# Kernel optimization log

Hardware: AMD Instinct MI355X
Metric: run time of the kernel (lower is better)

The kernel has to match this reference:

```python
import jax, jax.numpy as jnp
import numpy as np
from jax import lax

# hyperparams (match init_kwargs)
DIM = 192      # dim
QK = 192       # qk_dim
HEADS = 8
GS = 128       # group_size
MLP = 384      # mlp_dim
M = 64         # num_tokens
B, H, W = 4, 128, 128


def setup_inputs() -> dict:
    key = jax.random.key(0)
    ks = jax.random.split(key, 12)
    def n(k, sh, sc=0.02):
        return jax.random.normal(k, sh, dtype=jnp.float32) * sc
    return {
        "x": n(ks[0], (B, DIM, H, W), 1.0),
        "ln_g": jnp.ones((DIM,), jnp.float32),
        "ln_b": jnp.zeros((DIM,), jnp.float32),
        "Wq": n(ks[1], (DIM, QK)),
        "Wk": n(ks[2], (DIM, QK)),
        "Wv": n(ks[3], (DIM, DIM)),
        "Wproj": n(ks[4], (DIM, DIM)),
        "Wkg": n(ks[5], (DIM, QK)),      # IRCA global-key projection of means
        "Wvg": n(ks[6], (DIM, DIM)),     # IRCA global-value projection of means
        "means": n(ks[7], (M, DIM), 1.0),  # token dictionary buffer
        "Wconv": n(ks[8], (DIM, DIM)),   # 1x1 conv (no bias) as matrix
        "mlp_ln_g": jnp.ones((DIM,), jnp.float32),
        "mlp_ln_b": jnp.zeros((DIM,), jnp.float32),
        "W_fc1": n(ks[9], (DIM, MLP)),
        "dw": n(ks[10], (MLP, 1, 3, 3)),  # depthwise 3x3 in ConvFFN
        "W_fc2": n(ks[11], (MLP, DIM)),
    }


def _ln(x, g, b, eps=1e-5):
    mu = x.mean(-1, keepdims=True)
    var = ((x - mu) ** 2).mean(-1, keepdims=True)
    return (x - mu) * lax.rsqrt(var + eps) * g + b


def _attn(q, k, v):
    scale = q.shape[-1] ** -0.5
    s = jnp.einsum('...qd,...kd->...qk', q, k) * scale
    p = jax.nn.softmax(s, axis=-1)
    return jnp.einsum('...qk,...kd->...qd', p, v)


def reference(x, ln_g, ln_b, Wq, Wk, Wv, Wproj, Wkg, Wvg, means,
              Wconv, mlp_ln_g, mlp_ln_b, W_fc1, dw, W_fc2):
    b, C, h, w = x.shape
    N = h * w
    xt = x.reshape(b, C, N).transpose(0, 2, 1)          # b n c
    residual = xt
    xn = _ln(xt, ln_g, ln_b)

    # IRCA: per-head global K/V from the token dictionary (means)
    kg = (means @ Wkg).reshape(M, HEADS, QK // HEADS).transpose(1, 0, 2)   # h m dq
    vg = (means @ Wvg).reshape(M, HEADS, C // HEADS).transpose(1, 0, 2)    # h m dv

    # cluster assignment (no-grad): cosine sim to means, argsort by cluster id
    xs = lax.stop_gradient(xn)
    ms = lax.stop_gradient(means)
    xs_n = xs / (jnp.linalg.norm(xs, axis=-1, keepdims=True) + 1e-12)
    ms_n = ms / (jnp.linalg.norm(ms, axis=-1, keepdims=True) + 1e-12)
    belong = jnp.argmax(xs_n @ ms_n.T, axis=-1)          # b n
    idx = jnp.argsort(belong, axis=-1)                   # b n, cluster-sorted order

    # IASA: project, gather into cluster-sorted order
    q = jnp.take_along_axis(xn @ Wq, idx[:, :, None], axis=1)
    k = jnp.take_along_axis(xn @ Wk, idx[:, :, None], axis=1)
    v = jnp.take_along_axis(xn @ Wv, idx[:, :, None], axis=1)

    gs = min(N, GS)
    ng = (N + gs - 1) // gs
    pad_n = ng * gs - N
    pq = jnp.concatenate([q, q[:, N - pad_n:N][:, ::-1]], axis=1)
    pq = pq.reshape(b, ng, gs, HEADS, -1).transpose(0, 1, 3, 2, 4)  # b ng h gs dq

    def windows(t):
        tr = jnp.concatenate([t, t[:, N - pad_n - gs:N][:, ::-1]], axis=1)  # len ng*gs+gs
        t1 = tr[:, :ng * gs].reshape(b, ng, gs, -1)
        t2 = tr[:, gs:].reshape(b, ng, gs, -1)
        tw = jnp.concatenate([t1, t2], axis=2)           # b ng 2gs c
        return tw.reshape(b, ng, 2 * gs, HEADS, -1).transpose(0, 1, 3, 2, 4)

    kw, vw = windows(k), windows(v)
    out1 = _attn(pq, kw, vw)                             # local overlapping windows
    out2 = _attn(pq, kg[None, None], vg[None, None])     # global dictionary attention
    out = (out1 + out2).transpose(0, 1, 3, 2, 4).reshape(b, ng * gs, C)[:, :N]

    # scatter back to original token order (idx is a permutation)
    inv = jnp.argsort(idx, axis=-1)
    out = jnp.take_along_axis(out, inv[:, :, None], axis=1)
    out = (out @ Wproj) @ Wconv                           # proj + 1x1 conv (no bias)
    xt = residual + out

    # PreNorm ConvFFN: LN -> fc1 -> depthwise 3x3 -> GELU -> fc2, residual
    h1 = _ln(xt, mlp_ln_g, mlp_ln_b) @ W_fc1              # b n mlp
    himg = h1.transpose(0, 2, 1).reshape(b, MLP, h, w)
    dwc = lax.conv_general_dilated(himg, dw, (1, 1), 'SAME',
                                   feature_group_count=MLP,
                                   dimension_numbers=('NCHW', 'OIHW', 'NCHW'))
    h2 = jax.nn.gelu(dwc.reshape(b, MLP, N).transpose(0, 2, 1))
    xt = xt + h2 @ W_fc2
    return xt.transpose(0, 2, 1).reshape(b, C, h, w)
```

## Files before the change

### kernel.cpp

```cpp
#include <hip/hip_runtime.h>

using u16 = unsigned short;
using u32 = unsigned int;
typedef __attribute__((ext_vector_type(8))) short short8;
typedef __attribute__((ext_vector_type(4))) short s16x4;
typedef __attribute__((ext_vector_type(4))) float f32x4;
typedef __attribute__((ext_vector_type(2))) float f32x2;
typedef __attribute__((ext_vector_type(4))) u16 u16x4;
typedef __attribute__((ext_vector_type(4))) u32 u32x4;

constexpr int CB   = 4;
constexpr int CC   = 192;
constexpr int CN   = 16384;
constexpr int BN   = CB * CN;
constexpr int CMLP = 384;

__device__ __forceinline__ float b2f(u16 u){ return __uint_as_float(((u32)u) << 16); }
__device__ __forceinline__ u16 f2b(float f){
  u32 u = __float_as_uint(f);
  u32 r = (u + 0x7FFFu + ((u >> 16) & 1u)) >> 16;
  return (u16)r;
}
__device__ __forceinline__ short8 ld8(const u16* p) {
  s16x4 a = *(const s16x4*)p;
  s16x4 b = *(const s16x4*)(p + 4);
  short8 r;
  r[0]=a[0]; r[1]=a[1]; r[2]=a[2]; r[3]=a[3];
  r[4]=b[0]; r[5]=b[1]; r[6]=b[2]; r[7]=b[3];
  return r;
}
__device__ __forceinline__ u32 pk_bf16(float lo, float hi) {
  u32 r;
  asm("v_cvt_pk_bf16_f32 %0, %1, %2" : "=v"(r) : "v"(lo), "v"(hi));
  return r;
}
__device__ __forceinline__ float exp2_fast(float x) {
  float r;
  asm("v_exp_f32 %0, %1" : "=v"(r) : "v"(x));
  return r;
}
__device__ __forceinline__ void gl_lds16(const u16* g, u16* l) {
  __builtin_amdgcn_global_load_lds(
      (const __attribute__((address_space(1))) void*)(const void*)g,
      (__attribute__((address_space(3))) void*)(void*)l, 16, 0, 0);
}

template<int DOARG>
__global__ __launch_bounds__(256) void ln_k(const float* __restrict__ src,
    const float* __restrict__ gg, const float* __restrict__ bb, u16* __restrict__ out,
    const u16* __restrict__ msnT, int* __restrict__ belong)
{
  __shared__ float t[64 * 193];
  __shared__ float sg[192], sb[192];
  __shared__ float smu[64], srs[64];
  const int tid = threadIdx.x;
  const int blk = blockIdx.x;
  const int b = blk >> 8;
  const int n0 = (blk & 255) * 64;
  if (tid < 192) { sg[tid] = gg[tid]; sb[tid] = bb[tid]; }
  const size_t sbase = ((size_t)b * CC) * CN + n0;
  #pragma unroll
  for (int it = 0; it < 48; ++it) {
    int c = it * 4 + (tid >> 6);
    int tok = tid & 63;
    t[tok * 193 + c] = src[sbase + (size_t)c * CN + tok];
  }
  __syncthreads();
  {
    int tok = tid >> 2, sub = tid & 3;
    float s = 0.f, sq = 0.f;
    #pragma unroll
    for (int i = 0; i < 48; ++i) {
      float v = t[tok * 193 + sub * 48 + i];
      s += v; sq += v * v;
    }
    s  += __shfl_xor(s, 1);  s  += __shfl_xor(s, 2);
    sq += __shfl_xor(sq, 1); sq += __shfl_xor(sq, 2);
    float mu = s * (1.f / 192.f);
    float var = fmaxf(sq * (1.f / 192.f) - mu * mu, 0.f);
    float rs = rsqrtf(var + 1e-5f);
    if (sub == 0) { smu[tok] = mu; srs[tok] = rs; }
  }
  __syncthreads();
  const size_t obase = ((size_t)(b * CN + n0)) * CC;
  #pragma unroll
  for (int it = 0; it < 48; ++it) {
    int e = it * 256 + tid;
    int tk = e / 192, c = e % 192;
    float v = (t[tk * 193 + c] - smu[tk]) * srs[tk] * sg[c] + sb[c];
    out[obase + (size_t)tk * CC + c] = f2b(v);
  }

  if (DOARG) {
    const int wv = tid >> 6, lane = tid & 63;
    const int l15 = lane & 15, g4 = lane >> 4, q8 = g4 * 8;
    const int tok = wv * 16 + l15;
    const float mu = smu[tok], rs = srs[tok];
    short8 afm[6];
    #pragma unroll
    for (int ks = 0; ks < 6; ++ks) {
      u32x4 qq;
      #pragma unroll
      for (int j = 0; j < 4; ++j) {
        int c = ks * 32 + q8 + 2 * j;
        float v0 = (t[tok * 193 + c]     - mu) * rs * sg[c]     + sb[c];
        float v1 = (t[tok * 193 + c + 1] - mu) * rs * sg[c + 1] + sb[c + 1];
        qq[j] = pk_bf16(v0, v1);
      }
      afm[ks] = __builtin_bit_cast(short8, qq);
    }
    f32x4 sacc[4];
    #pragma unroll
    for (int ct = 0; ct < 4; ++ct) {
      sacc[ct] = 0.f;
      const u16* pM = msnT + (ct * 16 + l15) * 192 + q8;
      short8 mf[6];
      #pragma unroll
      for (int ks = 0; ks < 6; ++ks) mf[ks] = *(const short8*)(pM + ks * 32);
      #pragma unroll
      for (int ks = 0; ks < 6; ++ks)
        sacc[ct] = __builtin_amdgcn_mfma_f32_16x16x32_bf16(afm[ks], mf[ks], sacc[ct], 0, 0, 0);
    }
    #pragma unroll
    for (int r = 0; r < 4; ++r) {
      float bv = -3e38f; int bi = 1 << 30;
      #pragma unroll
      for (int ct = 0; ct < 4; ++ct) {
        float v = sacc[ct][r];
        int ci = ct * 16 + l15;
        if (v > bv || (v == bv && ci < bi)) { bv = v; bi = ci; }
      }
      #pragma unroll
      for (int d = 1; d < 16; d <<= 1) {
        float ov = __shfl_xor(bv, d);
        int   oi = __shfl_xor(bi, d);
        if (ov > bv || (ov == bv && oi < bi)) { bv = ov; bi = oi; }
      }
      if (l15 == 0) belong[b * CN + n0 + wv * 16 + g4 * 4 + r] = bi;
    }
  }
}

__global__ __launch_bounds__(192) void prep_means_k(const float* __restrict__ means,
    const float* __restrict__ Wkg, const float* __restrict__ Wvg,
    u16* __restrict__ msnT, float* __restrict__ kg, float* __restrict__ vg)
{
  __shared__ float sv[192];
  __shared__ float red[192];
  const int m = blockIdx.x, c = threadIdx.x;
  float v = means[m * 192 + c];
  sv[c] = v; red[c] = v * v;
  __syncthreads();
  for (int s = 96; s >= 3; s >>= 1) {
    if (c < s) red[c] += red[c + s];
    __syncthreads();
  }
  if (c == 0) red[0] = 1.f / (sqrtf(red[0] + red[1] + red[2]) + 1e-12f);
  __syncthreads();
  float scale = red[0];
  msnT[m * 192 + c] = f2b(v * scale);
  float a1 = 0.f, a2 = 0.f;
  for (int cc = 0; cc < 192; ++cc) {
    float mv = sv[cc];
    a1 += mv * Wkg[cc * 192 + c];
    a2 += mv * Wvg[cc * 192 + c];
  }
  int h = c / 24, d = c % 24;
  kg[h * (64 * 24) + m * 24 + d] = a1;
  vg[h * (64 * 24) + m * 24 + d] = a2;
}

__global__ __launch_bounds__(256) void wpcT_k(const float* __restrict__ Wp,
    const float* __restrict__ Wc, u16* __restrict__ WpcT)
{
  int e = blockIdx.x * 256 + threadIdx.x;
  if (e >= 192 * 192) return;
  int i = e / 192, j = e % 192;
  float a = 0.f;
  for (int k = 0; k < 192; ++k) a += Wp[i * 192 + k] * Wc[k * 192 + j];
  WpcT[j * 192 + i] = f2b(a);
}

__global__ __launch_bounds__(256) void wT_k(const float* __restrict__ W,
    u16* __restrict__ dst, int K, int NCsrc, int jcount)
{
  int e = blockIdx.x * 256 + threadIdx.x;
  if (e >= K * jcount) return;
  int j = e / K, k = e % K;
  dst[e] = f2b(W[k * NCsrc + j]);
}

enum { EP_QKV = 0, EP_RESID = 2, EP_H1 = 3, EP_FINAL = 4 };

template<int KTOT, int NCOLS, int EPI>
__global__ __launch_bounds__(256) void gemm3_k(const u16* __restrict__ A,
    const u16* __restrict__ Wt, const float* __restrict__ resid,
    void* __restrict__ outp, int astride,
    const float* __restrict__ g2, const float* __restrict__ b2, u16* __restrict__ ln2out)
{
  constexpr bool LNB = (EPI == EP_RESID);
  constexpr size_t SH_BYTES = LNB ? (size_t)(64 * 197 * 4) : (size_t)(64 * 192 * 2);
  __shared__ __attribute__((aligned(16))) char shraw[SH_BYTES];
  __shared__ float smu2[64], srs2[64];
  u16*   lA    = (u16*)shraw;
  float* lnbuf = (float*)shraw;
  constexpr int KC = KTOT / 192;
  constexpr int WCOLS = NCOLS / 4;
  constexpr int WCT = WCOLS / 16;
  constexpr int NACC = (KC == 2) ? WCT * 4 : 4;
  const int tid = threadIdx.x;
  const int row0 = blockIdx.y * 64;
  const int b = row0 >> 14;
  const int col0 = blockIdx.x * NCOLS;
  const int wv = tid >> 6, lane = tid & 63;
  const int l15 = lane & 15, g4 = lane >> 4, q8 = g4 * 8;
  const int colw = col0 + wv * WCOLS;

  f32x4 acc[NACC];
  #pragma unroll
  for (int i = 0; i < NACC; ++i) acc[i] = 0.f;

  #pragma unroll
  for (int kc = 0; kc < KC; ++kc) {
    if (kc) __syncthreads();
    #pragma unroll
    for (int j = 0; j < 6; ++j) {
      int C = (wv * 6 + j) * 64 + lane;
      int r = C / 24;
      int c = C - r * 24;
      const u16* gp = A + (size_t)(row0 + r) * astride + kc * 192 + c * 8;
      gl_lds16(gp, lA + (wv * 6 + j) * 512);
    }
    __syncthreads();
    short8 af[4][6];
    #pragma unroll
    for (int rt = 0; rt < 4; ++rt)
      #pragma unroll
      for (int ks = 0; ks < 6; ++ks)
        af[rt][ks] = *(const short8*)(lA + (rt * 16 + l15) * 192 + ks * 32 + q8);
    if (LNB) __syncthreads();

    #pragma unroll
    for (int jc = 0; jc < WCT; ++jc) {
      const u16* pW = Wt + (size_t)(colw + jc * 16 + l15) * KTOT + kc * 192 + q8;
      short8 wf[6];
      #pragma unroll
      for (int ks = 0; ks < 6; ++ks) wf[ks] = *(const short8*)(pW + ks * 32);
      #pragma unroll
      for (int ks = 0; ks < 6; ++ks)
        #pragma unroll
        for (int rt = 0; rt < 4; ++rt) {
          int ai = (KC == 2) ? jc * 4 + rt : rt;
          if (EPI == EP_FINAL || EPI == EP_RESID)
            acc[ai] = __builtin_amdgcn_mfma_f32_16x16x32_bf16(wf[ks], af[rt][ks], acc[ai], 0, 0, 0);
          else
            acc[ai] = __builtin_amdgcn_mfma_f32_16x16x32_bf16(af[rt][ks], wf[ks], acc[ai], 0, 0, 0);
        }

      if (KC == 1 && EPI == EP_QKV) {
        u16* o = (u16*)outp;
        int col = colw + jc * 16 + l15;
        #pragma unroll
        for (int rt = 0; rt < 4; ++rt) {
          int row = row0 + rt * 16 + g4 * 4;
          #pragma unroll
          for (int r = 0; r < 4; ++r)
            o[(size_t)(row + r) * 576 + col] = f2b(acc[rt][r]);
          acc[rt] = 0.f;
        }
      } else if (KC == 1 && EPI == EP_H1) {
        u16* o = (u16*)outp;
        int col = colw + jc * 16 + l15;
        #pragma unroll
        for (int rt = 0; rt < 4; ++rt) {
          int row = row0 + rt * 16 + g4 * 4;
          #pragma unroll
          for (int r = 0; r < 4; ++r)
            o[(size_t)(row + r) * CMLP + col] = f2b(acc[rt][r]);
          acc[rt] = 0.f;
        }
      } else if (KC == 1 && EPI == EP_RESID) {
        float* o = (float*)outp;
        #pragma unroll
        for (int rt = 0; rt < 4; ++rt) {
          int n = ((row0 + rt * 16) & 16383) + l15;
          #pragma unroll
          for (int r = 0; r < 4; ++r) {
            int col = colw + jc * 16 + g4 * 4 + r;
            size_t o2 = ((size_t)(b * CC + col)) * CN + n;
            float val = resid[o2] + acc[rt][r];
            o[o2] = val;
            lnbuf[(rt * 16 + l15) * 197 + col] = val;
          }
          acc[rt] = 0.f;
        }
      }
    }
  }

  if (EPI == EP_RESID) {
    __syncthreads();
    {
      int tok = tid >> 2, sub = tid & 3;
      float s = 0.f, sq = 0.f;
      #pragma unroll
      for (int i = 0; i < 48; ++i) {
        float v = lnbuf[tok * 197 + sub * 48 + i];
        s += v; sq += v * v;
      }
      s  += __shfl_xor(s, 1);  s  += __shfl_xor(s, 2);
      sq += __shfl_xor(sq, 1); sq += __shfl_xor(sq, 2);
      float mu = s * (1.f / 192.f);
      float var = fmaxf(sq * (1.f / 192.f) - mu * mu, 0.f);
      float rs = rsqrtf(var + 1e-5f);
      if (sub == 0) { smu2[tok] = mu; srs2[tok] = rs; }
    }
    __syncthreads();
    const size_t obase = (size_t)row0 * CC;
    #pragma unroll
    for (int it = 0; it < 48; ++it) {
      int e = it * 256 + tid;
      int tk = e / 192, c = e % 192;
      float v = (lnbuf[tk * 197 + c] - smu2[tk]) * srs2[tk] * g2[c] + b2[c];
      ln2out[obase + (size_t)tk * CC + c] = f2b(v);
    }
  } else if (EPI == EP_FINAL) {
    float* o = (float*)outp;
    #pragma unroll
    for (int jc = 0; jc < WCT; ++jc)
      #pragma unroll
      for (int tt = 0; tt < 4; ++tt) {
        int n = ((row0 + tt * 16) & 16383) + l15;
        #pragma unroll
        for (int r = 0; r < 4; ++r) {
          int outcol = colw + jc * 16 + g4 * 4 + r;
          size_t o2 = ((size_t)(b * CC + outcol)) * CN + n;
          o[o2] = resid[o2] + acc[jc * 4 + tt][r];
        }
      }
  }
}

__global__ __launch_bounds__(256) void hist_k(const int* __restrict__ belong, int* __restrict__ histG)
{
  __shared__ int h[64];
  int tid = threadIdx.x, blk = blockIdx.x;
  if (tid < 64) h[tid] = 0;
  __syncthreads();
  int c = belong[blk * 256 + tid];
  atomicAdd(&h[c], 1);
  __syncthreads();
  if (tid < 64) histG[blk * 64 + tid] = h[tid];
}

__global__ __launch_bounds__(64) void scan_k(const int* __restrict__ histG, int* __restrict__ chunkBase)
{
  int b = blockIdx.x, c = threadIdx.x;
  int tot = 0;
  for (int ch = 0; ch < 64; ++ch) tot += histG[(b * 64 + ch) * 64 + c];
  int inc = tot;
  for (int d = 1; d < 64; d <<= 1) {
    int v = __shfl_up(inc, d);
    if (c >= d) inc += v;
  }
  int run = inc - tot;
  for (int ch = 0; ch < 64; ++ch) {
    chunkBase[(b * 64 + ch) * 64 + c] = run;
    run += histG[(b * 64 + ch) * 64 + c];
  }
}

__global__ __launch_bounds__(256) void rank_k(const int* __restrict__ belong,
    const int* __restrict__ chunkBase, int* __restrict__ idx)
{
  __shared__ int WH[4][64];
  int tid = threadIdx.x, blk = blockIdx.x;
  int b = blk >> 6, chl = blk & 63;
  int wv = tid >> 6, lane = tid & 63;
  ((int*)WH)[tid] = 0;
  __syncthreads();
  int nl = chl * 256 + tid;
  int c = belong[blk * 256 + tid];
  int rank = 0;
  for (int m = 0; m < 64; ++m) {
    unsigned long long msk = __ballot(c == m);
    if (c == m) {
      rank = __popcll(msk & ((1ull << lane) - 1ull));
      if (rank == 0) WH[wv][m] = __popcll(msk);
    }
  }
  __syncthreads();
  int off = 0;
  #pragma unroll
  for (int w = 0; w < 3; ++w) if (w < wv) off += WH[w][c];
  int pos = chunkBase[(b * 64 + chl) * 64 + c] + off + rank;
  idx[b * CN + pos] = nl;
}

__global__ __launch_bounds__(256) void attn_k(u16* __restrict__ qkv,
    const float* __restrict__ kg, const float* __restrict__ vg,
    const int* __restrict__ idx)
{
  __shared__ __attribute__((aligned(16))) u16 sK[320 * 28];
  __shared__ __attribute__((aligned(16))) u16 sVT[25 * 340];
  __shared__ int sidx[256];
  const int g = blockIdx.x, h = blockIdx.y, b = blockIdx.z;
  const int tid = threadIdx.x;
  const int wave = tid >> 6, lane = tid & 63;
  const int l15 = lane & 15, g4 = lane >> 4;
  const int q8 = g4 * 8;
  const size_t base = (size_t)b * CN * 576;
  const float QSC = 0.20412414523193154f * 1.4426950408889634f;
  short8 z8 = {0,0,0,0,0,0,0,0};

  {
    int p = g * 128 + tid;
    if (p >= CN) p = 2 * CN - 1 - p;
    sidx[tid] = idx[b * CN + p];
  }
  for (int e = tid; e < 340; e += 256) sVT[24 * 340 + e] = 0x3F80;
  __syncthreads();

  #pragma unroll
  for (int it = 0; it < 8; ++it) {
    int e4 = (it * 256 + tid) * 4;
    if (e4 < 7680) {
      int r = e4 / 24, c = e4 % 24;
      if (r < 256) {
        int p = sidx[r];
        *(u16x4*)(sK + r * 28 + c) =
          *(const u16x4*)(qkv + base + (size_t)p * 576 + 192 + h * 24 + c);
      } else {
        const float* kp = kg + h * 1536 + (r - 256) * 24 + c;
        u16x4 o;
        o[0] = f2b(kp[0]); o[1] = f2b(kp[1]); o[2] = f2b(kp[2]); o[3] = f2b(kp[3]);
        *(u16x4*)(sK + r * 28 + c) = o;
      }
    }
  }
  #pragma unroll
  for (int it = 0; it < 8; ++it) {
    int e4 = (it * 256 + tid) * 4;
    if (e4 < 7680) {
      int kk = e4 / 24, c = e4 % 24;
      if (kk < 256) {
        int p = sidx[kk];
        u16x4 v = *(const u16x4*)(qkv + base + (size_t)p * 576 + 384 + h * 24 + c);
        sVT[(c + 0) * 340 + kk] = v[0];
        sVT[(c + 1) * 340 + kk] = v[1];
        sVT[(c + 2) * 340 + kk] = v[2];
        sVT[(c + 3) * 340 + kk] = v[3];
      } else {
        const float* vp = vg + h * 1536 + (kk - 256) * 24 + c;
        sVT[(c + 0) * 340 + kk] = f2b(vp[0]);
        sVT[(c + 1) * 340 + kk] = f2b(vp[1]);
        sVT[(c + 2) * 340 + kk] = f2b(vp[2]);
        sVT[(c + 3) * 340 + kk] = f2b(vp[3]);
      }
    }
  }

  short8 qf[2];
  #pragma unroll
  for (int rt = 0; rt < 2; ++rt) {
    int qrow = sidx[wave * 32 + rt * 16 + l15];
    if (g4 < 3) {
      short8 raw = ld8(qkv + base + (size_t)qrow * 576 + h * 24 + q8);
      u32x4 qq;
      #pragma unroll
      for (int j = 0; j < 4; ++j) {
        float lo = b2f((u16)raw[2 * j]) * QSC;
        float hi = b2f((u16)raw[2 * j + 1]) * QSC;
        qq[j] = pk_bf16(lo, hi);
      }
      qf[rt] = __builtin_bit_cast(short8, qq);
    } else {
      qf[rt] = z8;
    }
  }
  __syncthreads();

  f32x4 O1[2][2], O2[2][2];
  #pragma unroll
  for (int rt = 0; rt < 2; ++rt)
    #pragma unroll
    for (int ct2 = 0; ct2 < 2; ++ct2) { O1[rt][ct2] = 0.f; O2[rt][ct2] = 0.f; }

  const int srcLo = ((lane & 16) << 1) + l15;
  const int srcHi = srcLo + 16;
  const bool hiSel = lane >= 32;
  f32x4 zz = 0.f;

  auto do_tile = [&](int ktile, f32x4 (*O)[2]) {
    short8 aK[4];
    #pragma unroll
    for (int ct = 0; ct < 4; ++ct)
      aK[ct] = (g4 < 3) ? ld8(sK + (ktile + ct * 16 + l15) * 28 + q8) : z8;
    short8 bV[2][2];
    #pragma unroll
    for (int kc = 0; kc < 2; ++kc)
      #pragma unroll
      for (int ct2 = 0; ct2 < 2; ++ct2) {
        int vrow = ct2 * 16 + l15;
        bV[kc][ct2] = (vrow < 25) ? ld8(sVT + vrow * 340 + ktile + kc * 32 + q8) : z8;
      }
    #pragma unroll
    for (int rt = 0; rt < 2; ++rt) {
      f32x4 p[4];
      #pragma unroll
      for (int ct = 0; ct < 4; ++ct)
        p[ct] = __builtin_amdgcn_mfma_f32_16x16x32_bf16(aK[ct], qf[rt], zz, 0, 0, 0);
      #pragma unroll
      for (int ct = 0; ct < 4; ++ct)
        #pragma unroll
        for (int r = 0; r < 4; ++r)
          p[ct][r] = exp2_fast(p[ct][r]);
      #pragma unroll
      for (int kc = 0; kc < 2; ++kc) {
        u32 wA0 = pk_bf16(p[kc * 2][0], p[kc * 2][1]);
        u32 wA1 = pk_bf16(p[kc * 2][2], p[kc * 2][3]);
        u32 wB0 = pk_bf16(p[kc * 2 + 1][0], p[kc * 2 + 1][1]);
        u32 wB1 = pk_bf16(p[kc * 2 + 1][2], p[kc * 2 + 1][3]);
        u32 a0 = (u32)__shfl((int)wA0, srcLo), a1 = (u32)__shfl((int)wA1, srcLo);
        u32 a2 = (u32)__shfl((int)wA0, srcHi), a3 = (u32)__shfl((int)wA1, srcHi);
        u32 b0 = (u32)__shfl((int)wB0, srcLo), b1 = (u32)__shfl((int)wB1, srcLo);
        u32 b2 = (u32)__shfl((int)wB0, srcHi), b3 = (u32)__shfl((int)wB1, srcHi);
        u32x4 fr;
        fr[0] = hiSel ? b0 : a0; fr[1] = hiSel ? b1 : a1;
        fr[2] = hiSel ? b2 : a2; fr[3] = hiSel ? b3 : a3;
        short8 aP = __builtin_bit_cast(short8, fr);
        #pragma unroll
        for (int ct2 = 0; ct2 < 2; ++ct2)
          O[rt][ct2] = __builtin_amdgcn_mfma_f32_16x16x32_bf16(aP, bV[kc][ct2], O[rt][ct2], 0, 0, 0);
      }
    }
  };

  do_tile(0,   O1);
  do_tile(64,  O1);
  do_tile(128, O1);
  do_tile(192, O1);
  do_tile(256, O2);

  const int lsrc = (lane & 48) + 8;
  #pragma unroll
  for (int rt = 0; rt < 2; ++rt) {
    #pragma unroll
    for (int r = 0; r < 4; ++r) {
      float s1 = __shfl(O1[rt][1][r], lsrc);
      float s2 = __shfl(O2[rt][1][r], lsrc);
      float i1 = 1.f / s1;
      float i2 = 1.f / s2;
      int tok = sidx[wave * 32 + rt * 16 + g4 * 4 + r];
      #pragma unroll
      for (int ct2 = 0; ct2 < 2; ++ct2) {
        int d = ct2 * 16 + l15;
        if (d < 24) {
          float v = O1[rt][ct2][r] * i1 + O2[rt][ct2][r] * i2;
          qkv[base + (size_t)tok * 576 + h * 24 + d] = f2b(v);
        }
      }
    }
  }
}

__global__ __launch_bounds__(256) void conv_k(const u16* __restrict__ h1,
    const float* __restrict__ dw, u16* __restrict__ h2g)
{
  __shared__ float t[1156 * 10];
  __shared__ float sdw[72];
  const int tile = blockIdx.x;
  const int jg = blockIdx.y;
  const int bb = blockIdx.z;
  const int y0 = (tile >> 2) * 32, x0 = (tile & 3) * 32;
  const int tid = threadIdx.x;
  if (tid < 72) sdw[tid] = dw[jg * 72 + tid];
  #pragma unroll
  for (int it = 0; it < 5; ++it) {
    int e = it * 256 + tid;
    if (e < 1156) {
      int yy = e / 34 - 1 + y0, xx = e % 34 - 1 + x0;
      float v[8];
      if (yy >= 0 && yy < 128 && xx >= 0 && xx < 128) {
        short8 raw = *(const short8*)(h1 + ((size_t)(bb * CN + yy * 128 + xx)) * CMLP + jg * 8);
        #pragma unroll
        for (int c = 0; c < 8; ++c) v[c] = b2f((u16)raw[c]);
      } else {
        #pragma unroll
        for (int c = 0; c < 8; ++c) v[c] = 0.f;
      }
      #pragma unroll
      for (int c = 0; c < 8; c += 2) {
        f32x2 p; p[0] = v[c]; p[1] = v[c + 1];
        *(f32x2*)(t + e * 10 + c) = p;
      }
    }
  }
  __syncthreads();
  float acc[4][8];
  #pragma unroll
  for (int px = 0; px < 4; ++px)
    #pragma unroll
    for (int c = 0; c < 8; ++c) acc[px][c] = 0.f;
  #pragma unroll
  for (int k = 0; k < 9; ++k) {
    const int dy = k / 3, dx = k % 3;
    float w[8];
    #pragma unroll
    for (int c = 0; c < 8; ++c) w[c] = sdw[c * 9 + k];
    #pragma unroll
    for (int px = 0; px < 4; ++px) {
      int idx2 = px * 256 + tid;
      int oy = idx2 >> 5, ox = idx2 & 31;
      const float* vp = t + ((oy + dy) * 34 + ox + dx) * 10;
      #pragma unroll
      for (int c = 0; c < 8; ++c) acc[px][c] += vp[c] * w[c];
    }
  }
  #pragma unroll
  for (int px = 0; px < 4; ++px) {
    int idx2 = px * 256 + tid;
    int oy = idx2 >> 5, ox = idx2 & 31;
    short8 o;
    #pragma unroll
    for (int c = 0; c < 8; ++c) {
      float a = acc[px][c];
      float u = 1.5957691216057308f * (a + 0.044715f * a * a * a);
      float gel = a / (1.f + __expf(-u));
      o[c] = (short)f2b(gel);
    }
    *(short8*)(h2g + ((size_t)(bb * CN + (y0 + oy) * 128 + x0 + ox)) * CMLP + jg * 8) = o;
  }
}

extern "C" void kernel_launch(void* const* d_in, const int* in_sizes, int n_in,
                              void* d_out, int out_size, void* d_ws, size_t ws_size,
                              hipStream_t stream)
{
  const float* x     = (const float*)d_in[0];
  const float* ln_g  = (const float*)d_in[1];
  const float* ln_b  = (const float*)d_in[2];
  const float* Wq    = (const float*)d_in[3];
  const float* Wk    = (const float*)d_in[4];
  const float* Wv    = (const float*)d_in[5];
  const float* Wproj = (const float*)d_in[6];
  const float* Wkg   = (const float*)d_in[7];
  const float* Wvg   = (const float*)d_in[8];
  const float* means = (const float*)d_in[9];
  const float* Wconv = (const float*)d_in[10];
  const float* mlp_g = (const float*)d_in[11];
  const float* mlp_b = (const float*)d_in[12];
  const float* Wfc1  = (const float*)d_in[13];
  const float* dw    = (const float*)d_in[14];
  const float* Wfc2  = (const float*)d_in[15];
  float* out = (float*)d_out;
  (void)in_sizes; (void)n_in; (void)out_size; (void)ws_size;

  char* ws = (char*)d_ws;
  size_t off = 0;
  auto alloc = [&](size_t sz) { void* p = ws + off; off += (sz + 255) & ~(size_t)255; return p; };
  u16*  xn    = (u16*)alloc((size_t)BN * 192 * 2);
  u16*  qkv   = (u16*)alloc((size_t)BN * 576 * 2);
  float* xt2  = (float*)alloc((size_t)BN * 192 * 4);
  u16*  h2g   = (u16*)alloc((size_t)BN * 384 * 2);
  u16*  msnT  = (u16*)alloc(64 * 192 * 2);
  u16*  WqkvT = (u16*)alloc(576 * 192 * 2);
  u16*  WpcT  = (u16*)alloc(192 * 192 * 2);
  u16*  Wfc1T = (u16*)alloc(384 * 192 * 2);
  u16*  Wfc2T = (u16*)alloc(192 * 384 * 2);
  float* kg   = (float*)alloc(8 * 64 * 24 * 4);
  float* vg   = (float*)alloc(8 * 64 * 24 * 4);
  int*  belong = (int*)alloc(BN * 4);
  int*  idxb   = (int*)alloc(BN * 4);
  int*  histG  = (int*)alloc(256 * 64 * 4);
  int*  chunkBase = (int*)alloc(256 * 64 * 4);
  u16* ln2 = xn;
  u16* h1  = qkv;

  prep_means_k<<<64, 192, 0, stream>>>(means, Wkg, Wvg, msnT, kg, vg);
  wpcT_k<<<144, 256, 0, stream>>>(Wproj, Wconv, WpcT);
  wT_k<<<144, 256, 0, stream>>>(Wq, WqkvT + 0,             192, 192, 192);
  wT_k<<<144, 256, 0, stream>>>(Wk, WqkvT + 192 * 192,     192, 192, 192);
  wT_k<<<144, 256, 0, stream>>>(Wv, WqkvT + 2 * 192 * 192, 192, 192, 192);
  wT_k<<<288, 256, 0, stream>>>(Wfc1, Wfc1T, 192, 384, 384);
  wT_k<<<288, 256, 0, stream>>>(Wfc2, Wfc2T, 384, 192, 192);

  ln_k<1><<<1024, 256, 0, stream>>>(x, ln_g, ln_b, xn, msnT, belong);
  hist_k<<<256, 256, 0, stream>>>(belong, histG);
  scan_k<<<4, 64, 0, stream>>>(histG, chunkBase);
  rank_k<<<256, 256, 0, stream>>>(belong, chunkBase, idxb);
  gemm3_k<192, 576, EP_QKV><<<dim3(1, 1024), 256, 0, stream>>>(xn, WqkvT, nullptr, qkv, 192, nullptr, nullptr, nullptr);
  attn_k<<<dim3(128, 8, 4), 256, 0, stream>>>(qkv, kg, vg, idxb);
  gemm3_k<192, 192, EP_RESID><<<dim3(1, 1024), 256, 0, stream>>>(qkv, WpcT, x, xt2, 576, mlp_g, mlp_b, ln2);
  gemm3_k<192, 384, EP_H1><<<dim3(1, 1024), 256, 0, stream>>>(ln2, Wfc1T, nullptr, h1, 192, nullptr, nullptr, nullptr);
  conv_k<<<dim3(16, 48, 4), 256, 0, stream>>>(h1, dw, h2g);
  gemm3_k<384, 192, EP_FINAL><<<dim3(1, 1024), 256, 0, stream>>>(h2g, Wfc2T, xt2, out, 384, nullptr, nullptr, nullptr);
}
```

Before: 339.9 us.

## Merge weight-prep kernels, store residual in bf16, shrink attention LDS padding

Merges the five weight transpose/convert launches and the proj-conv product into one wprep_k launch, saving launch overhead. The intermediate residual xt2 is now stored as bf16 instead of fp32, halving its write in the resid GEMM and its read in the final GEMM, at some cost in precision on the residual path. The attention kernel drops LDS row padding (28→24, 340→332) and stores sidx as u16, which shrinks shared memory but may bring back bank conflicts.

```diff
diff --git a/kernel.cpp b/kernel.cpp
--- a/kernel.cpp
+++ b/kernel.cpp
@@ -170,31 +170,60 @@
   vg[h * (64 * 24) + m * 24 + d] = a2;
 }
 
-__global__ __launch_bounds__(256) void wpcT_k(const float* __restrict__ Wp,
-    const float* __restrict__ Wc, u16* __restrict__ WpcT)
-{
-  int e = blockIdx.x * 256 + threadIdx.x;
-  if (e >= 192 * 192) return;
-  int i = e / 192, j = e % 192;
-  float a = 0.f;
-  for (int k = 0; k < 192; ++k) a += Wp[i * 192 + k] * Wc[k * 192 + j];
-  WpcT[j * 192 + i] = f2b(a);
-}
-
-__global__ __launch_bounds__(256) void wT_k(const float* __restrict__ W,
-    u16* __restrict__ dst, int K, int NCsrc, int jcount)
-{
-  int e = blockIdx.x * 256 + threadIdx.x;
-  if (e >= K * jcount) return;
-  int j = e / K, k = e % K;
-  dst[e] = f2b(W[k * NCsrc + j]);
+__global__ __launch_bounds__(256) void wprep_k(
+    const float* __restrict__ Wp, const float* __restrict__ Wc, u16* __restrict__ WpcT,
+    const float* __restrict__ Wq, const float* __restrict__ Wk, const float* __restrict__ Wv,
+    u16* __restrict__ WqkvT,
+    const float* __restrict__ Wfc1, u16* __restrict__ Wfc1T,
+    const float* __restrict__ Wfc2, u16* __restrict__ Wfc2T)
+{
+  int blk = blockIdx.x;
+  int tid = threadIdx.x;
+  if (blk < 144) {
+    int e = blk * 256 + tid;
+    if (e < 192 * 192) {
+      int i = e / 192, j = e % 192;
+      float a = 0.f;
+      for (int k = 0; k < 192; ++k) a += Wp[i * 192 + k] * Wc[k * 192 + j];
+      WpcT[j * 192 + i] = f2b(a);
+    }
+    return;
+  }
+  blk -= 144;
+  if (blk < 432) {
+    int which = blk / 144;
+    int e = (blk % 144) * 256 + tid;
+    const float* W = (which == 0) ? Wq : (which == 1) ? Wk : Wv;
+    if (e < 192 * 192) {
+      int j = e / 192, k = e % 192;
+      WqkvT[which * 192 * 192 + e] = f2b(W[k * 192 + j]);
+    }
+    return;
+  }
+  blk -= 432;
+  if (blk < 288) {
+    int e = blk * 256 + tid;
+    if (e < 192 * 384) {
+      int j = e / 192, k = e % 192;
+      Wfc1T[e] = f2b(Wfc1[k * 384 + j]);
+    }
+    return;
+  }
+  blk -= 288;
+  {
+    int e = blk * 256 + tid;
+    if (e < 384 * 192) {
+      int j = e / 384, k = e % 384;
+      Wfc2T[e] = f2b(Wfc2[k * 192 + j]);
+    }
+  }
 }
 
 enum { EP_QKV = 0, EP_RESID = 2, EP_H1 = 3, EP_FINAL = 4 };
 
 template<int KTOT, int NCOLS, int EPI>
 __global__ __launch_bounds__(256) void gemm3_k(const u16* __restrict__ A,
-    const u16* __restrict__ Wt, const float* __restrict__ resid,
+    const u16* __restrict__ Wt, const void* __restrict__ residp,
     void* __restrict__ outp, int astride,
     const float* __restrict__ g2, const float* __restrict__ b2, u16* __restrict__ ln2out)
 {
@@ -280,7 +309,8 @@
           acc[rt] = 0.f;
         }
       } else if (KC == 1 && EPI == EP_RESID) {
-        float* o = (float*)outp;
+        const float* resid = (const float*)residp;
+        u16* o = (u16*)outp;
         #pragma unroll
         for (int rt = 0; rt < 4; ++rt) {
           int n = ((row0 + rt * 16) & 16383) + l15;
@@ -289,7 +319,7 @@
             int col = colw + jc * 16 + g4 * 4 + r;
             size_t o2 = ((size_t)(b * CC + col)) * CN + n;
             float val = resid[o2] + acc[rt][r];
-            o[o2] = val;
+            o[o2] = f2b(val);
             lnbuf[(rt * 16 + l15) * 197 + col] = val;
           }
           acc[rt] = 0.f;
@@ -325,6 +355,7 @@
       ln2out[obase + (size_t)tk * CC + c] = f2b(v);
     }
   } else if (EPI == EP_FINAL) {
+    const u16* resid = (const u16*)residp;
     float* o = (float*)outp;
     #pragma unroll
     for (int jc = 0; jc < WCT; ++jc)
@@ -335,7 +366,7 @@
         for (int r = 0; r < 4; ++r) {
           int outcol = colw + jc * 16 + g4 * 4 + r;
           size_t o2 = ((size_t)(b * CC + outcol)) * CN + n;
-          o[o2] = resid[o2] + acc[jc * 4 + tt][r];
+          o[o2] = b2f(resid[o2]) + acc[jc * 4 + tt][r];
         }
       }
   }
@@ -401,9 +432,9 @@
     const float* __restrict__ kg, const float* __restrict__ vg,
     const int* __restrict__ idx)
 {
-  __shared__ __attribute__((aligned(16))) u16 sK[320 * 28];
-  __shared__ __attribute__((aligned(16))) u16 sVT[25 * 340];
-  __shared__ int sidx[256];
+  __shared__ __attribute__((aligned(16))) u16 sK[320 * 24];
+  __shared__ __attribute__((aligned(16))) u16 sVT[25 * 332];
+  __shared__ u16 sidx[256];
   const int g = blockIdx.x, h = blockIdx.y, b = blockIdx.z;
   const int tid = threadIdx.x;
   const int wave = tid >> 6, lane = tid & 63;
@@ -416,9 +447,9 @@
   {
     int p = g * 128 + tid;
     if (p >= CN) p = 2 * CN - 1 - p;
-    sidx[tid] = idx[b * CN + p];
-  }
-  for (int e = tid; e < 340; e += 256) sVT[24 * 340 + e] = 0x3F80;
+    sidx[tid] = (u16)idx[b * CN + p];
+  }
+  for (int e = tid; e < 332; e += 256) sVT[24 * 332 + e] = 0x3F80;
   __syncthreads();
 
   #pragma unroll
@@ -428,13 +459,13 @@
       int r = e4 / 24, c = e4 % 24;
       if (r < 256) {
         int p = sidx[r];
-        *(u16x4*)(sK + r * 28 + c) =
+        *(u16x4*)(sK + r * 24 + c) =
           *(const u16x4*)(qkv + base + (size_t)p * 576 + 192 + h * 24 + c);
       } else {
         const float* kp = kg + h * 1536 + (r - 256) * 24 + c;
         u16x4 o;
         o[0] = f2b(kp[0]); o[1] = f2b(kp[1]); o[2] = f2b(kp[2]); o[3] = f2b(kp[3]);
-        *(u16x4*)(sK + r * 28 + c) = o;
+        *(u16x4*)(sK + r * 24 + c) = o;
       }
     }
   }
@@ -446,16 +477,16 @@
       if (kk < 256) {
         int p = sidx[kk];
         u16x4 v = *(const u16x4*)(qkv + base + (size_t)p * 576 + 384 + h * 24 + c);
-        sVT[(c + 0) * 340 + kk] = v[0];
-        sVT[(c + 1) * 340 + kk] = v[1];
-        sVT[(c + 2) * 340 + kk] = v[2];
-        sVT[(c + 3) * 340 + kk] = v[3];
+        sVT[(c + 0) * 332 + kk] = v[0];
+        sVT[(c + 1) * 332 + kk] = v[1];
+        sVT[(c + 2) * 332 + kk] = v[2];
+        sVT[(c + 3) * 332 + kk] = v[3];
       } else {
         const float* vp = vg + h * 1536 + (kk - 256) * 24 + c;
-        sVT[(c + 0) * 340 + kk] = f2b(vp[0]);
-        sVT[(c + 1) * 340 + kk] = f2b(vp[1]);
-        sVT[(c + 2) * 340 + kk] = f2b(vp[2]);
-        sVT[(c + 3) * 340 + kk] = f2b(vp[3]);
+        sVT[(c + 0) * 332 + kk] = f2b(vp[0]);
+        sVT[(c + 1) * 332 + kk] = f2b(vp[1]);
+        sVT[(c + 2) * 332 + kk] = f2b(vp[2]);
+        sVT[(c + 3) * 332 + kk] = f2b(vp[3]);
       }
     }
   }
@@ -495,14 +526,14 @@
     short8 aK[4];
     #pragma unroll
     for (int ct = 0; ct < 4; ++ct)
-      aK[ct] = (g4 < 3) ? ld8(sK + (ktile + ct * 16 + l15) * 28 + q8) : z8;
+      aK[ct] = (g4 < 3) ? ld8(sK + (ktile + ct * 16 + l15) * 24 + q8) : z8;
     short8 bV[2][2];
     #pragma unroll
     for (int kc = 0; kc < 2; ++kc)
       #pragma unroll
       for (int ct2 = 0; ct2 < 2; ++ct2) {
         int vrow = ct2 * 16 + l15;
-        bV[kc][ct2] = (vrow < 25) ? ld8(sVT + vrow * 340 + ktile + kc * 32 + q8) : z8;
+        bV[kc][ct2] = (vrow < 25) ? ld8(sVT + vrow * 332 + ktile + kc * 32 + q8) : z8;
       }
     #pragma unroll
     for (int rt = 0; rt < 2; ++rt) {
@@ -661,7 +692,7 @@
   auto alloc = [&](size_t sz) { void* p = ws + off; off += (sz + 255) & ~(size_t)255; return p; };
   u16*  xn    = (u16*)alloc((size_t)BN * 192 * 2);
   u16*  qkv   = (u16*)alloc((size_t)BN * 576 * 2);
-  float* xt2  = (float*)alloc((size_t)BN * 192 * 4);
+  u16*  xt2   = (u16*)alloc((size_t)BN * 192 * 2);
   u16*  h2g   = (u16*)alloc((size_t)BN * 384 * 2);
   u16*  msnT  = (u16*)alloc(64 * 192 * 2);
   u16*  WqkvT = (u16*)alloc(576 * 192 * 2);
@@ -678,12 +709,8 @@
   u16* h1  = qkv;
 
   prep_means_k<<<64, 192, 0, stream>>>(means, Wkg, Wvg, msnT, kg, vg);
-  wpcT_k<<<144, 256, 0, stream>>>(Wproj, Wconv, WpcT);
-  wT_k<<<144, 256, 0, stream>>>(Wq, WqkvT + 0,             192, 192, 192);
-  wT_k<<<144, 256, 0, stream>>>(Wk, WqkvT + 192 * 192,     192, 192, 192);
-  wT_k<<<144, 256, 0, stream>>>(Wv, WqkvT + 2 * 192 * 192, 192, 192, 192);
-  wT_k<<<288, 256, 0, stream>>>(Wfc1, Wfc1T, 192, 384, 384);
-  wT_k<<<288, 256, 0, stream>>>(Wfc2, Wfc2T, 384, 192, 192);
+  wprep_k<<<1152, 256, 0, stream>>>(Wproj, Wconv, WpcT, Wq, Wk, Wv, WqkvT,
+                                    Wfc1, Wfc1T, Wfc2, Wfc2T);
 
   ln_k<1><<<1024, 256, 0, stream>>>(x, ln_g, ln_b, xn, msnT, belong);
   hist_k<<<256, 256, 0, stream>>>(belong, histG);
```

New measurement: 321.7 us. 1.06x faster.
